# Optimization experiments

Hardware: AMD Instinct MI355X
Metric: run time of the kernel (lower is better)

The kernel has to match this reference:

```python
import jax, jax.numpy as jnp
import numpy as np

B, F_IN, N, T = 32, 64, 512, 64


def setup_inputs() -> dict:
    key = jax.random.key(0)
    ks = jax.random.split(key, 6)
    s = 0.05  # small init scale so sigmoid/softmax stay in a sane range
    return {
        "x": jax.random.normal(ks[0], (B, F_IN, N, T), dtype=jnp.float32),
        "U1": jax.random.normal(ks[1], (N,), dtype=jnp.float32) * s,
        "U2": jax.random.normal(ks[2], (N, F_IN), dtype=jnp.float32) * s,
        "U3": jax.random.normal(ks[3], (F_IN,), dtype=jnp.float32) * s,
        "be": jax.random.normal(ks[4], (1, T, T), dtype=jnp.float32) * s,
        "Ve": jax.random.normal(ks[5], (T, T), dtype=jnp.float32) * s,
    }


def reference(x, U1, U2, U3, be, Ve):
    # x: (B, F, N, T)
    # lhs = U2 @ (x^T @ U1): (B, N, T)
    t1 = jnp.einsum("bfnt,n->bft", x, U1)          # (B, F, T)
    lhs = jnp.einsum("nf,bft->bnt", U2, t1)        # (B, N, T)
    # rhs = sum_f U3[f] * x[:, f]: (B, N, T)
    rhs = jnp.einsum("f,bfnt->bnt", U3, x)         # (B, N, T)
    # product = lhs^T @ rhs: (B, T, T)
    product = jnp.einsum("bnt,bns->bts", lhs, rhs)
    # E = Ve @ sigmoid(product + be): (B, T, T)
    E = jnp.einsum("ts,bsu->btu", Ve, jax.nn.sigmoid(product + be))
    # softmax over dim=1 (rows of E), then x_flat @ A, reshape back
    A = jax.nn.softmax(E, axis=1)                  # (B, T, T)
    out = jnp.einsum("bfnt,bts->bfns", x, A)       # (B, F, N, T)
    return out
```

## Files before the change

kernel.cpp:

```cpp
#include <hip/hip_runtime.h>
#include <hip/hip_bf16.h>

#define B_ 32
#define F_ 64
#define N_ 512
#define T_ 64

typedef __attribute__((ext_vector_type(8))) short bf16x8;
typedef __attribute__((ext_vector_type(4))) float f32x4;

__device__ __forceinline__ unsigned short f2bf(float f) {
  union { float f; unsigned int u; } v; v.f = f;
  unsigned int u = v.u;
  unsigned int r = (u + 0x7FFFu + ((u >> 16) & 1u)) >> 16;
  return (unsigned short)r;
}

__global__ __launch_bounds__(256) void k1_reduce(const float* __restrict__ x,
    const float* __restrict__ U1, const float* __restrict__ U3,
    float* __restrict__ t1part, float* __restrict__ rhs) {
  const int b = blockIdx.x;
  const int nc = blockIdx.y;
  const int n0 = nc * 16;
  const int tid = threadIdx.x;
  const int w = tid >> 6;
  const int lane = tid & 63;
  const int n_sub = lane >> 4;
  const int t0 = (lane & 15) * 4;

  __shared__ float lds[4096];

  const float* xb = x + (size_t)b * (F_ * (size_t)N_ * T_);

  float u1c[4];
#pragma unroll
  for (int i = 0; i < 4; ++i) u1c[i] = U1[n0 + n_sub * 4 + i];

  float racc[4][4];
#pragma unroll
  for (int i = 0; i < 4; ++i)
#pragma unroll
    for (int k = 0; k < 4; ++k) racc[i][k] = 0.f;

#pragma unroll
  for (int j = 0; j < 16; ++j) {
    const int f = w * 16 + j;
    const float u3 = U3[f];
    const float* xf = xb + (size_t)f * (N_ * T_) + (size_t)(n0 + n_sub * 4) * T_ + t0;
    float p0 = 0.f, p1 = 0.f, p2 = 0.f, p3 = 0.f;
#pragma unroll
    for (int i = 0; i < 4; ++i) {
      const float4 v = *(const float4*)(xf + i * T_);
      racc[i][0] += u3 * v.x; racc[i][1] += u3 * v.y;
      racc[i][2] += u3 * v.z; racc[i][3] += u3 * v.w;
      p0 += u1c[i] * v.x; p1 += u1c[i] * v.y;
      p2 += u1c[i] * v.z; p3 += u1c[i] * v.w;
    }
    p0 += __shfl_xor(p0, 16); p0 += __shfl_xor(p0, 32);
    p1 += __shfl_xor(p1, 16); p1 += __shfl_xor(p1, 32);
    p2 += __shfl_xor(p2, 16); p2 += __shfl_xor(p2, 32);
    p3 += __shfl_xor(p3, 16); p3 += __shfl_xor(p3, 32);
    if (lane < 16) {
      float4 st; st.x = p0; st.y = p1; st.z = p2; st.w = p3;
      *(float4*)&t1part[((size_t)(b * 32 + nc) * 64 + f) * 64 + t0] = st;
    }
  }

#pragma unroll
  for (int i = 0; i < 4; ++i) {
    float4 st; st.x = racc[i][0]; st.y = racc[i][1]; st.z = racc[i][2]; st.w = racc[i][3];
    *(float4*)&lds[w * 1024 + (n_sub * 4 + i) * 64 + t0] = st;
  }
  __syncthreads();
#pragma unroll
  for (int q = 0; q < 4; ++q) {
    const int idx = q * 256 + tid;
    const float s = lds[idx] + lds[1024 + idx] + lds[2048 + idx] + lds[3072 + idx];
    rhs[((size_t)b * N_ + n0 + (idx >> 6)) * T_ + (idx & 63)] = s;
  }
}

__global__ __launch_bounds__(256) void k2_w(const float* __restrict__ rhs,
    const float* __restrict__ U2, float* __restrict__ wpart) {
  const int b = blockIdx.x;
  const int c = blockIdx.y;
  const int n0 = c * 64;
  const int tid = threadIdx.x;
  const int s = tid & 63;
  const int fg = tid >> 6;
  __shared__ float lu2[64 * 64];
  __shared__ float lr[64 * 64];
#pragma unroll
  for (int q = 0; q < 16; ++q) {
    const int idx = q * 256 + tid;
    const int i = idx >> 6, cc = idx & 63;
    lu2[idx] = U2[(size_t)(n0 + i) * F_ + cc];
    lr[idx] = rhs[((size_t)b * N_ + n0 + i) * T_ + cc];
  }
  __syncthreads();
  float acc[16];
#pragma unroll
  for (int j = 0; j < 16; ++j) acc[j] = 0.f;
  for (int i = 0; i < 64; ++i) {
    const float rv = lr[i * 64 + s];
#pragma unroll
    for (int j = 0; j < 16; ++j) acc[j] += lu2[i * 64 + fg * 16 + j] * rv;
  }
#pragma unroll
  for (int j = 0; j < 16; ++j)
    wpart[(size_t)(b * 8 + c) * 4096 + (size_t)(fg * 16 + j) * 64 + s] = acc[j];
}

__global__ __launch_bounds__(256) void kred(const float* __restrict__ t1part,
    const float* __restrict__ wpart, float* __restrict__ t1, float* __restrict__ wbf) {
  const int gid = blockIdx.x * 256 + threadIdx.x;
  if (gid < 131072) {
    const int b = gid >> 12, idx = gid & 4095;
    const float* p = t1part + (size_t)b * 32 * 4096 + idx;
    float sum = 0.f;
#pragma unroll
    for (int c = 0; c < 32; ++c) sum += p[c * 4096];
    t1[gid] = sum;
  } else {
    const int g = gid - 131072;
    const int b = g >> 12, idx = g & 4095;
    const float* p = wpart + (size_t)b * 8 * 4096 + idx;
    float sum = 0.f;
#pragma unroll
    for (int c = 0; c < 8; ++c) sum += p[c * 4096];
    wbf[g] = sum;
  }
}

__global__ __launch_bounds__(256) void k3_attn(const float* __restrict__ t1,
    const float* __restrict__ wbuf, const float* __restrict__ be,
    const float* __restrict__ Ve, float* __restrict__ Amat) {
  const int b = blockIdx.x;
  const int tid = threadIdx.x;
  const int lane = tid & 63;
  const int tg = tid >> 6;
  __shared__ float bufA[64 * 65];
  __shared__ float bufB[64 * 65];
  __shared__ float red[2][4][64];
#pragma unroll
  for (int q = 0; q < 16; ++q) {
    const int idx = q * 256 + tid;
    const int r = idx >> 6, c = idx & 63;
    bufA[r * 65 + c] = t1[(size_t)b * 4096 + idx];
    bufB[r * 65 + c] = wbuf[(size_t)b * 4096 + idx];
  }
  __syncthreads();
  float prod[16];
#pragma unroll
  for (int j = 0; j < 16; ++j) prod[j] = 0.f;
  for (int f = 0; f < 64; ++f) {
    const float wv = bufB[f * 65 + lane];
#pragma unroll
    for (int j = 0; j < 16; ++j) prod[j] += bufA[f * 65 + tg * 16 + j] * wv;
  }
  __syncthreads();
#pragma unroll
  for (int j = 0; j < 16; ++j) {
    const int tt = tg * 16 + j;
    const float v = prod[j] + be[tt * 64 + lane];
    bufA[tt * 65 + lane] = 1.f / (1.f + __expf(-v));
  }
#pragma unroll
  for (int q = 0; q < 16; ++q) {
    const int idx = q * 256 + tid;
    bufB[(idx >> 6) * 65 + (idx & 63)] = Ve[idx];
  }
  __syncthreads();
  float E[16];
#pragma unroll
  for (int j = 0; j < 16; ++j) E[j] = 0.f;
  for (int s = 0; s < 64; ++s) {
    const float sv = bufA[s * 65 + lane];
#pragma unroll
    for (int j = 0; j < 16; ++j) E[j] += bufB[(tg * 16 + j) * 65 + s] * sv;
  }
  float m = E[0];
#pragma unroll
  for (int j = 1; j < 16; ++j) m = fmaxf(m, E[j]);
  red[0][tg][lane] = m;
  __syncthreads();
  m = fmaxf(fmaxf(red[0][0][lane], red[0][1][lane]),
            fmaxf(red[0][2][lane], red[0][3][lane]));
  float se = 0.f;
  float ex[16];
#pragma unroll
  for (int j = 0; j < 16; ++j) { ex[j] = __expf(E[j] - m); se += ex[j]; }
  red[1][tg][lane] = se;
  __syncthreads();
  const float gs = red[1][0][lane] + red[1][1][lane] + red[1][2][lane] + red[1][3][lane];
  const float inv = 1.f / gs;
#pragma unroll
  for (int j = 0; j < 16; ++j) {
    const int tt = tg * 16 + j;
    Amat[(size_t)b * 4096 + tt * 64 + lane] = ex[j] * inv;
  }
}

__global__ __launch_bounds__(256) void k4_out(const float* __restrict__ x,
    const float* __restrict__ Amat, float* __restrict__ out) {
  const int b = blockIdx.x;
  const int chunk = blockIdx.y;
  const int tid = threadIdx.x;
  const int wv = tid >> 6;
  const int l = tid & 63;
  __shared__ float lA[64 * 65];
  const float* Ab = Amat + (size_t)b * 4096;
#pragma unroll
  for (int q = 0; q < 16; ++q) {
    const int idx = q * 256 + tid;
    lA[(idx >> 6) * 65 + (idx & 63)] = Ab[idx];
  }
  __syncthreads();

  const int krow0 = (l >> 4) * 8;
  const int colb = l & 15;
  bf16x8 Bf[4][2];
#pragma unroll
  for (int nt = 0; nt < 4; ++nt)
#pragma unroll
    for (int kh = 0; kh < 2; ++kh) {
      bf16x8 fr;
#pragma unroll
      for (int j = 0; j < 8; ++j) {
        const int k = kh * 32 + krow0 + j;
        fr[j] = (short)f2bf(lA[k * 65 + nt * 16 + colb]);
      }
      Bf[nt][kh] = fr;
    }

  const float* Xb = x + (size_t)b * (F_ * (size_t)N_ * T_);
  float* Ob = out + (size_t)b * (F_ * (size_t)N_ * T_);
  const int rl = l & 15;
  const int c0 = (l >> 4) * 8;

  for (int it = 0; it < 4; ++it) {
    const int tile = chunk * 16 + wv * 4 + it;
    const int r = tile * 16 + rl;
    const float* xr = Xb + (size_t)r * T_;
    const float4 v0 = *(const float4*)(xr + c0);
    const float4 v1 = *(const float4*)(xr + c0 + 4);
    const float4 v2 = *(const float4*)(xr + 32 + c0);
    const float4 v3 = *(const float4*)(xr + 32 + c0 + 4);
    bf16x8 a0, a1;
    a0[0] = (short)f2bf(v0.x); a0[1] = (short)f2bf(v0.y);
    a0[2] = (short)f2bf(v0.z); a0[3] = (short)f2bf(v0.w);
    a0[4] = (short)f2bf(v1.x); a0[5] = (short)f2bf(v1.y);
    a0[6] = (short)f2bf(v1.z); a0[7] = (short)f2bf(v1.w);
    a1[0] = (short)f2bf(v2.x); a1[1] = (short)f2bf(v2.y);
    a1[2] = (short)f2bf(v2.z); a1[3] = (short)f2bf(v2.w);
    a1[4] = (short)f2bf(v3.x); a1[5] = (short)f2bf(v3.y);
    a1[6] = (short)f2bf(v3.z); a1[7] = (short)f2bf(v3.w);

    const int rowb = tile * 16 + (l >> 4) * 4;
#pragma unroll
    for (int nt = 0; nt < 4; ++nt) {
      f32x4 c = {0.f, 0.f, 0.f, 0.f};
      c = __builtin_amdgcn_mfma_f32_16x16x32_bf16(a0, Bf[nt][0], c, 0, 0, 0);
      c = __builtin_amdgcn_mfma_f32_16x16x32_bf16(a1, Bf[nt][1], c, 0, 0, 0);
#pragma unroll
      for (int j = 0; j < 4; ++j)
        Ob[(size_t)(rowb + j) * T_ + nt * 16 + colb] = c[j];
    }
  }
}

extern "C" void kernel_launch(void* const* d_in, const int* in_sizes, int n_in,
                              void* d_out, int out_size, void* d_ws, size_t ws_size,
                              hipStream_t stream) {
  const float* x  = (const float*)d_in[0];
  const float* U1 = (const float*)d_in[1];
  const float* U2 = (const float*)d_in[2];
  const float* U3 = (const float*)d_in[3];
  const float* be = (const float*)d_in[4];
  const float* Ve = (const float*)d_in[5];
  float* out = (float*)d_out;
  float* ws = (float*)d_ws;

  float* t1part = ws;
  float* rhs    = t1part + 4194304;
  float* wpart  = rhs + 1048576;
  float* t1     = wpart + 1048576;
  float* wbf    = t1 + 131072;
  float* Amat   = wbf + 131072;

  k1_reduce<<<dim3(32, 32), 256, 0, stream>>>(x, U1, U3, t1part, rhs);
  k2_w<<<dim3(32, 8), 256, 0, stream>>>(rhs, U2, wpart);
  kred<<<1024, 256, 0, stream>>>(t1part, wpart, t1, wbf);
  k3_attn<<<32, 256, 0, stream>>>(t1, wbf, be, Ve, Amat);
  k4_out<<<dim3(32, 128), 256, 0, stream>>>(x, Amat, out);
}
```

Baseline: 198.7 us.

## Stage x tiles through per-wave LDS double buffer with async global-to-LDS loads

The first reduction kernel no longer loads x straight into registers. Each wave now copies one f-slice at a time into its own double-buffered LDS ring using global_load_lds, prefetching the next slice while it computes on the current one, and synchronises with explicit s_waitcnt. The goal is to overlap global memory latency with the FMA work and reduce register pressure in this bandwidth-bound pass. The cost is that only one slice is ever in flight, where the fully unrolled loop could previously issue many loads ahead. Correctness also relies on hand-written vmcnt counts, which can be disturbed by the interleaved global stores.

```diff
diff --git a/kernel.cpp b/kernel.cpp
--- a/kernel.cpp
+++ b/kernel.cpp
@@ -14,6 +14,13 @@
   unsigned int u = v.u;
   unsigned int r = (u + 0x7FFFu + ((u >> 16) & 1u)) >> 16;
   return (unsigned short)r;
+}
+
+__device__ __forceinline__ void gl_lds16(const float* g, float* l) {
+  __builtin_amdgcn_global_load_lds(
+      (const __attribute__((address_space(1))) unsigned int*)(g),
+      (__attribute__((address_space(3))) unsigned int*)(l),
+      16, 0, 0);
 }
 
 __global__ __launch_bounds__(256) void k1_reduce(const float* __restrict__ x,
@@ -28,9 +35,9 @@
   const int n_sub = lane >> 4;
   const int t0 = (lane & 15) * 4;
 
-  __shared__ float lds[4096];
-
-  const float* xb = x + (size_t)b * (F_ * (size_t)N_ * T_);
+  __shared__ float ring[4][2][1024];
+
+  const float* fbase = x + ((size_t)(b * F_ + w * 16) * N_ + n0) * T_;
 
   float u1c[4];
 #pragma unroll
@@ -42,15 +49,33 @@
 #pragma unroll
     for (int k = 0; k < 4; ++k) racc[i][k] = 0.f;
 
-#pragma unroll
+  {
+    const float* s = fbase;
+    float* l = &ring[w][0][0];
+#pragma unroll
+    for (int c = 0; c < 4; ++c) gl_lds16(s + c * 256 + lane * 4, l + c * 256);
+  }
+
+#pragma unroll 2
   for (int j = 0; j < 16; ++j) {
+    const int buf = j & 1;
+    if (j < 15) {
+      const float* s = fbase + (size_t)(j + 1) * (N_ * T_);
+      float* l = &ring[w][buf ^ 1][0];
+#pragma unroll
+      for (int c = 0; c < 4; ++c) gl_lds16(s + c * 256 + lane * 4, l + c * 256);
+      asm volatile("s_waitcnt vmcnt(4)" ::: "memory");
+    } else {
+      asm volatile("s_waitcnt vmcnt(0)" ::: "memory");
+    }
+    __builtin_amdgcn_sched_barrier(0);
+
     const int f = w * 16 + j;
     const float u3 = U3[f];
-    const float* xf = xb + (size_t)f * (N_ * T_) + (size_t)(n0 + n_sub * 4) * T_ + t0;
     float p0 = 0.f, p1 = 0.f, p2 = 0.f, p3 = 0.f;
 #pragma unroll
     for (int i = 0; i < 4; ++i) {
-      const float4 v = *(const float4*)(xf + i * T_);
+      const float4 v = *(const float4*)&ring[w][buf][(n_sub * 4 + i) * 64 + t0];
       racc[i][0] += u3 * v.x; racc[i][1] += u3 * v.y;
       racc[i][2] += u3 * v.z; racc[i][3] += u3 * v.w;
       p0 += u1c[i] * v.x; p1 += u1c[i] * v.y;
@@ -69,13 +94,13 @@
 #pragma unroll
   for (int i = 0; i < 4; ++i) {
     float4 st; st.x = racc[i][0]; st.y = racc[i][1]; st.z = racc[i][2]; st.w = racc[i][3];
-    *(float4*)&lds[w * 1024 + (n_sub * 4 + i) * 64 + t0] = st;
+    *(float4*)&ring[w][0][(n_sub * 4 + i) * 64 + t0] = st;
   }
   __syncthreads();
 #pragma unroll
   for (int q = 0; q < 4; ++q) {
     const int idx = q * 256 + tid;
-    const float s = lds[idx] + lds[1024 + idx] + lds[2048 + idx] + lds[3072 + idx];
+    const float s = ring[0][0][idx] + ring[1][0][idx] + ring[2][0][idx] + ring[3][0][idx];
     rhs[((size_t)b * N_ + n0 + (idx >> 6)) * T_ + (idx & 63)] = s;
   }
 }
```

Result: faster. 192.9 us (-2.9%).

## Drop shuffle reduction in k1, store per-lane t1 partials; split k4 launches reversed

Applied to the files above, without the earlier changes.

k1 no longer reduces t1 partials across the four n_sub lane groups with cross-lane shuffles. Every lane now writes its own float4 partial, which quadruples the t1part workspace, and kred sums four extra strided entries per element. The x loads in k1 are also batched into a register buffer before the arithmetic. k4 is split into four launches that process batches in reverse order, likely so the most recently read x slices are still in cache. The cost is more global write traffic for the partials and more launch overhead.

```diff
diff --git a/kernel.cpp b/kernel.cpp
--- a/kernel.cpp
+++ b/kernel.cpp
@@ -28,7 +28,7 @@
   const int n_sub = lane >> 4;
   const int t0 = (lane & 15) * 4;
 
-  __shared__ float lds[4096];
+  __shared__ float lds[4][1024];
 
   const float* xb = x + (size_t)b * (F_ * (size_t)N_ * T_);
 
@@ -41,41 +41,40 @@
   for (int i = 0; i < 4; ++i)
 #pragma unroll
     for (int k = 0; k < 4; ++k) racc[i][k] = 0.f;
+
+  float* tp = t1part + ((size_t)(b * 32 + nc) * 64) * 256 + lane * 4;
 
 #pragma unroll
   for (int j = 0; j < 16; ++j) {
     const int f = w * 16 + j;
     const float u3 = U3[f];
     const float* xf = xb + (size_t)f * (N_ * T_) + (size_t)(n0 + n_sub * 4) * T_ + t0;
+    float4 buf[4];
+#pragma unroll
+    for (int i = 0; i < 4; ++i) buf[i] = *(const float4*)(xf + i * T_);
     float p0 = 0.f, p1 = 0.f, p2 = 0.f, p3 = 0.f;
 #pragma unroll
     for (int i = 0; i < 4; ++i) {
-      const float4 v = *(const float4*)(xf + i * T_);
+      const float4 v = buf[i];
       racc[i][0] += u3 * v.x; racc[i][1] += u3 * v.y;
       racc[i][2] += u3 * v.z; racc[i][3] += u3 * v.w;
       p0 += u1c[i] * v.x; p1 += u1c[i] * v.y;
       p2 += u1c[i] * v.z; p3 += u1c[i] * v.w;
     }
-    p0 += __shfl_xor(p0, 16); p0 += __shfl_xor(p0, 32);
-    p1 += __shfl_xor(p1, 16); p1 += __shfl_xor(p1, 32);
-    p2 += __shfl_xor(p2, 16); p2 += __shfl_xor(p2, 32);
-    p3 += __shfl_xor(p3, 16); p3 += __shfl_xor(p3, 32);
-    if (lane < 16) {
-      float4 st; st.x = p0; st.y = p1; st.z = p2; st.w = p3;
-      *(float4*)&t1part[((size_t)(b * 32 + nc) * 64 + f) * 64 + t0] = st;
-    }
+    float4 st; st.x = p0; st.y = p1; st.z = p2; st.w = p3;
+    *(float4*)(tp + (size_t)f * 256) = st;
   }
 
 #pragma unroll
   for (int i = 0; i < 4; ++i) {
     float4 st; st.x = racc[i][0]; st.y = racc[i][1]; st.z = racc[i][2]; st.w = racc[i][3];
-    *(float4*)&lds[w * 1024 + (n_sub * 4 + i) * 64 + t0] = st;
+    *(float4*)&lds[w][(n_sub * 4 + i) * 64 + t0] = st;
   }
   __syncthreads();
 #pragma unroll
   for (int q = 0; q < 4; ++q) {
     const int idx = q * 256 + tid;
-    const float s = lds[idx] + lds[1024 + idx] + lds[2048 + idx] + lds[3072 + idx];
+    const float s = lds[0][idx] + lds[1][idx] + lds[2][idx] + lds[3][idx];
     rhs[((size_t)b * N_ + n0 + (idx >> 6)) * T_ + (idx & 63)] = s;
   }
 }
@@ -115,11 +114,16 @@
     const float* __restrict__ wpart, float* __restrict__ t1, float* __restrict__ wbf) {
   const int gid = blockIdx.x * 256 + threadIdx.x;
   if (gid < 131072) {
-    const int b = gid >> 12, idx = gid & 4095;
-    const float* p = t1part + (size_t)b * 32 * 4096 + idx;
+    const int b = gid >> 12;
+    const int f = (gid >> 6) & 63;
+    const int t = gid & 63;
+    const float* p = t1part + ((size_t)(b * 32) * 64 + f) * 256 + t;
     float sum = 0.f;
-#pragma unroll
-    for (int c = 0; c < 32; ++c) sum += p[c * 4096];
+#pragma unroll 4
+    for (int nc = 0; nc < 32; ++nc) {
+      const float* q = p + (size_t)nc * (64 * 256);
+      sum += q[0] + q[64] + q[128] + q[192];
+    }
     t1[gid] = sum;
   } else {
     const int g = gid - 131072;
@@ -202,8 +206,8 @@
 }
 
 __global__ __launch_bounds__(256) void k4_out(const float* __restrict__ x,
-    const float* __restrict__ Amat, float* __restrict__ out) {
-  const int b = blockIdx.x;
+    const float* __restrict__ Amat, float* __restrict__ out, int b0) {
+  const int b = b0 + blockIdx.x;
   const int chunk = blockIdx.y;
   const int tid = threadIdx.x;
   const int wv = tid >> 6;
@@ -282,7 +286,7 @@
   float* ws = (float*)d_ws;
 
   float* t1part = ws;
-  float* rhs    = t1part + 4194304;
+  float* rhs    = t1part + 16777216;
   float* wpart  = rhs + 1048576;
   float* t1     = wpart + 1048576;
   float* wbf    = t1 + 131072;
@@ -292,5 +296,8 @@
   k2_w<<<dim3(32, 8), 256, 0, stream>>>(rhs, U2, wpart);
   kred<<<1024, 256, 0, stream>>>(t1part, wpart, t1, wbf);
   k3_attn<<<32, 256, 0, stream>>>(t1, wbf, be, Ve, Amat);
-  k4_out<<<dim3(32, 128), 256, 0, stream>>>(x, Amat, out);
-}
+  k4_out<<<dim3(8, 128), 256, 0, stream>>>(x, Amat, out, 24);
+  k4_out<<<dim3(8, 128), 256, 0, stream>>>(x, Amat, out, 16);
+  k4_out<<<dim3(8, 128), 256, 0, stream>>>(x, Amat, out, 8);
+  k4_out<<<dim3(8, 128), 256, 0, stream>>>(x, Amat, out, 0);
+}
```

Result: slower. 242.1 us (+21.8%).
